# Kernel optimization log

Measured on AMD Instinct MI355X. Metric: run time of the kernel, lower is better.

The kernel has to match this reference:

```python
import jax, jax.numpy as jnp
import numpy as np

NUM_HEADS = 12

def setup_inputs() -> dict:
    key = jax.random.key(0)
    ks = jax.random.split(key, 4)
    B, N, C = 64, 512, 768
    x = jax.random.normal(ks[0], (B, N, C), dtype=jnp.float32)
    qkv_w = jax.random.normal(ks[1], (3 * C, C), dtype=jnp.float32) * 0.02
    proj_w = jax.random.normal(ks[2], (C, C), dtype=jnp.float32) * 0.02
    proj_b = jnp.zeros((C,), dtype=jnp.float32)
    bias_table = jax.random.normal(ks[3], (2 * N - 1, NUM_HEADS), dtype=jnp.float32) * 0.02
    return {"x": x, "qkv_w": qkv_w, "proj_w": proj_w, "proj_b": proj_b, "bias_table": bias_table}

def reference(x, qkv_w, proj_w, proj_b, bias_table):
    B, N, C = x.shape
    H = NUM_HEADS
    hd = C // H
    scale = hd ** (-0.5)
    # qkv projection (no bias): [B,N,3C] -> [3,B,H,N,hd]
    qkv = (x @ qkv_w.T).reshape(B, N, 3, H, hd)
    qkv = jnp.transpose(qkv, (2, 0, 3, 1, 4))
    q, k, v = qkv[0], qkv[1], qkv[2]
    # relative position bias: rel index in [0, 2N-2]
    coords = jnp.arange(N)
    rel = coords[:, None] - coords[None, :] + (N - 1)  # [N,N]
    bias = jnp.transpose(bias_table[rel], (2, 0, 1))   # [H,N,N]
    attn = jnp.einsum('bhnd,bhmd->bhnm', q, k) * scale + bias[None]
    attn = jax.nn.softmax(attn, axis=-1)
    out = jnp.einsum('bhnm,bhmd->bhnd', attn, v)       # [B,H,N,hd]
    out = jnp.transpose(out, (0, 2, 1, 3)).reshape(B, N, C)
    return out @ proj_w.T + proj_b
```

## Files before the change

kernel.cpp:

```cpp
#include <hip/hip_runtime.h>
#include <hip/hip_bf16.h>

#define DI static __device__ __forceinline__

typedef __attribute__((ext_vector_type(8), may_alias)) short short8;
typedef __attribute__((ext_vector_type(4), may_alias)) short short4a;
typedef __attribute__((ext_vector_type(4), may_alias)) float floatx4a;
typedef __attribute__((ext_vector_type(4))) float floatx4;

constexpr int Bsz = 64, Nseq = 512, Cdim = 768, NH = 12, HD = 64;
constexpr int QS = Bsz * NH * Nseq * HD;
constexpr float SCALE = 0.125f;

DI ushort f2bf(float f) {
  union { float f; unsigned u; } v; v.f = f;
  unsigned r = v.u + 0x7FFF + ((v.u >> 16) & 1);
  return (ushort)(r >> 16);
}
DI float bf2f(ushort u) {
  union { unsigned u; float f; } v; v.u = ((unsigned)u) << 16;
  return v.f;
}

__global__ void cvt8(const float* __restrict__ s, ushort* __restrict__ d, int n) {
  int i = (blockIdx.x * 256 + threadIdx.x) * 8;
  if (i >= n) return;
  floatx4a a = *(const floatx4a*)(s + i);
  floatx4a b = *(const floatx4a*)(s + i + 4);
  short8 r;
  r[0] = (short)f2bf(a[0]); r[1] = (short)f2bf(a[1]);
  r[2] = (short)f2bf(a[2]); r[3] = (short)f2bf(a[3]);
  r[4] = (short)f2bf(b[0]); r[5] = (short)f2bf(b[1]);
  r[6] = (short)f2bf(b[2]); r[7] = (short)f2bf(b[3]);
  *(short8*)(d + i) = r;
}
__global__ void cvt1(const float* __restrict__ s, ushort* __restrict__ d, int n) {
  int i = blockIdx.x * 256 + threadIdx.x;
  if (i < n) d[i] = f2bf(s[i]);
}

__global__ __launch_bounds__(256) void qkv_gemm(
    const ushort* __restrict__ x, const ushort* __restrict__ w,
    ushort* __restrict__ qo, ushort* __restrict__ ko, ushort* __restrict__ vo)
{
  __shared__ __align__(16) ushort As[128 * 72];
  __shared__ __align__(16) ushort Ws[128 * 72];
  const int bn = blockIdx.x;
  const int bm = blockIdx.y;
  const int t = threadIdx.x;
  const int wv = t >> 6, ln = t & 63, lq = ln >> 4, lm = ln & 15;
  const int wm = wv >> 1, wn = wv & 1;

  floatx4 acc[4][4];
  #pragma unroll
  for (int i = 0; i < 4; ++i)
    #pragma unroll
    for (int j = 0; j < 4; ++j) acc[i][j] = (floatx4)0.f;

  for (int kt = 0; kt < Cdim / 64; ++kt) {
    #pragma unroll
    for (int i = 0; i < 4; ++i) {
      int id = t + 256 * i;
      int r = id >> 3, c = (id & 7) << 3;
      *(short8*)&As[r * 72 + c] =
          *(const short8*)&x[(size_t)(bm * 128 + r) * Cdim + kt * 64 + c];
      *(short8*)&Ws[r * 72 + c] =
          *(const short8*)&w[(size_t)(bn * 128 + r) * Cdim + kt * 64 + c];
    }
    __syncthreads();
    #pragma unroll
    for (int ks = 0; ks < 2; ++ks) {
      short8 af[4], bfr[4];
      #pragma unroll
      for (int i = 0; i < 4; ++i)
        af[i] = *(const short8*)&As[(wm * 64 + i * 16 + lm) * 72 + ks * 32 + lq * 8];
      #pragma unroll
      for (int j = 0; j < 4; ++j)
        bfr[j] = *(const short8*)&Ws[(wn * 64 + j * 16 + lm) * 72 + ks * 32 + lq * 8];
      #pragma unroll
      for (int i = 0; i < 4; ++i)
        #pragma unroll
        for (int j = 0; j < 4; ++j)
          acc[i][j] = __builtin_amdgcn_mfma_f32_16x16x32_bf16(af[i], bfr[j], acc[i][j], 0, 0, 0);
    }
    __syncthreads();
  }

  const int cbase = bn * 128 + wn * 64;
  const int which = cbase / Cdim;
  const int h = (cbase % Cdim) >> 6;
  #pragma unroll
  for (int i = 0; i < 4; ++i) {
    int gm0 = bm * 128 + wm * 64 + i * 16 + lq * 4;
    int b = gm0 >> 9, ns0 = gm0 & 511;
    #pragma unroll
    for (int j = 0; j < 4; ++j) {
      int d = j * 16 + lm;
      if (which == 2) {
        short4a v4;
        #pragma unroll
        for (int r = 0; r < 4; ++r) v4[r] = (short)f2bf(acc[i][j][r]);
        *(short4a*)&vo[(size_t)((b * NH + h) * HD + d) * Nseq + ns0] = v4;
      } else {
        ushort* outp = which == 0 ? qo : ko;
        #pragma unroll
        for (int r = 0; r < 4; ++r)
          outp[(size_t)((b * NH + h) * Nseq + ns0 + r) * HD + d] = f2bf(acc[i][j][r]);
      }
    }
  }
}

__global__ __launch_bounds__(256) void attn_kernel(
    const ushort* __restrict__ q, const ushort* __restrict__ k,
    const ushort* __restrict__ vt, const ushort* __restrict__ bt,
    ushort* __restrict__ ao)
{
  __shared__ __align__(16) ushort Qs[64 * 72];
  __shared__ __align__(16) ushort Ks[64 * 72];
  __shared__ __align__(16) ushort Vs[64 * 72];
  __shared__ __align__(16) ushort Ps[64 * 72];
  __shared__ float biasLds[128];
  const int blk = blockIdx.x;
  const int bh = blk % (Bsz * NH);
  const int qt = blk / (Bsz * NH);
  const int h = bh % NH, b = bh / NH;
  const int t = threadIdx.x;
  const int wv = t >> 6, ln = t & 63, lq = ln >> 4, lm = ln & 15;
  const size_t base = (size_t)bh * (Nseq * HD);

  #pragma unroll
  for (int i = 0; i < 2; ++i) {
    int id = t + 256 * i;
    int r = id >> 3, c = (id & 7) << 3;
    *(short8*)&Qs[r * 72 + c] =
        *(const short8*)&q[base + (size_t)(qt * 64 + r) * HD + c];
  }

  floatx4 o[4];
  #pragma unroll
  for (int i = 0; i < 4; ++i) o[i] = (floatx4)0.f;
  float mrow[4], lrow[4];
  #pragma unroll
  for (int r = 0; r < 4; ++r) { mrow[r] = -1e30f; lrow[r] = 0.f; }

  for (int kt = 0; kt < Nseq / 64; ++kt) {
    #pragma unroll
    for (int i = 0; i < 2; ++i) {
      int id = t + 256 * i;
      int r = id >> 3, c = (id & 7) << 3;
      *(short8*)&Ks[r * 72 + c] =
          *(const short8*)&k[base + (size_t)(kt * 64 + r) * HD + c];
      *(short8*)&Vs[r * 72 + c] =
          *(const short8*)&vt[base + (size_t)r * Nseq + kt * 64 + c];
    }
    if (t < 127) biasLds[t] = bf2f(bt[(qt * 64 - kt * 64 + 448 + t) * NH + h]);
    __syncthreads();

    floatx4 s[4];
    #pragma unroll
    for (int cb = 0; cb < 4; ++cb) s[cb] = (floatx4)0.f;
    #pragma unroll
    for (int ks = 0; ks < 2; ++ks) {
      short8 a = *(const short8*)&Qs[(wv * 16 + lm) * 72 + ks * 32 + lq * 8];
      #pragma unroll
      for (int cb = 0; cb < 4; ++cb) {
        short8 bfr = *(const short8*)&Ks[(cb * 16 + lm) * 72 + ks * 32 + lq * 8];
        s[cb] = __builtin_amdgcn_mfma_f32_16x16x32_bf16(a, bfr, s[cb], 0, 0, 0);
      }
    }

    float pvals[4][4];
    #pragma unroll
    for (int r = 0; r < 4; ++r) {
      int row_in = wv * 16 + lq * 4 + r;
      float sv[4];
      float vmax = -1e30f;
      #pragma unroll
      for (int cb = 0; cb < 4; ++cb) {
        int col_in = cb * 16 + lm;
        float bias = biasLds[row_in - col_in + 63];
        sv[cb] = s[cb][r] * SCALE + bias;
        vmax = fmaxf(vmax, sv[cb]);
      }
      #pragma unroll
      for (int off = 8; off; off >>= 1) vmax = fmaxf(vmax, __shfl_xor(vmax, off));
      float mnew = fmaxf(mrow[r], vmax);
      float alpha = __expf(mrow[r] - mnew);
      float rsum = 0.f;
      #pragma unroll
      for (int cb = 0; cb < 4; ++cb) {
        float p = __expf(sv[cb] - mnew);
        pvals[cb][r] = p;
        rsum += p;
      }
      #pragma unroll
      for (int off = 8; off; off >>= 1) rsum += __shfl_xor(rsum, off);
      lrow[r] = lrow[r] * alpha + rsum;
      mrow[r] = mnew;
      #pragma unroll
      for (int db = 0; db < 4; ++db) o[db][r] *= alpha;
    }

    #pragma unroll
    for (int cb = 0; cb < 4; ++cb)
      #pragma unroll
      for (int r = 0; r < 4; ++r)
        Ps[(wv * 16 + lq * 4 + r) * 72 + cb * 16 + lm] = f2bf(pvals[cb][r]);

    __syncthreads();

    #pragma unroll
    for (int ks = 0; ks < 2; ++ks) {
      short8 a = *(const short8*)&Ps[(wv * 16 + lm) * 72 + ks * 32 + lq * 8];
      #pragma unroll
      for (int db = 0; db < 4; ++db) {
        short8 bfr = *(const short8*)&Vs[(db * 16 + lm) * 72 + ks * 32 + lq * 8];
        o[db] = __builtin_amdgcn_mfma_f32_16x16x32_bf16(a, bfr, o[db], 0, 0, 0);
      }
    }
    __syncthreads();
  }

  #pragma unroll
  for (int r = 0; r < 4; ++r) {
    int qi = qt * 64 + wv * 16 + lq * 4 + r;
    float inv = 1.f / lrow[r];
    #pragma unroll
    for (int db = 0; db < 4; ++db) {
      int d = db * 16 + lm;
      ao[(size_t)(b * Nseq + qi) * Cdim + h * HD + d] = f2bf(o[db][r] * inv);
    }
  }
}

__global__ __launch_bounds__(256) void proj_gemm(
    const ushort* __restrict__ a, const ushort* __restrict__ w,
    const ushort* __restrict__ pb, float* __restrict__ out)
{
  __shared__ __align__(16) ushort As[128 * 72];
  __shared__ __align__(16) ushort Ws[128 * 72];
  const int bn = blockIdx.x;
  const int bm = blockIdx.y;
  const int t = threadIdx.x;
  const int wv = t >> 6, ln = t & 63, lq = ln >> 4, lm = ln & 15;
  const int wm = wv >> 1, wn = wv & 1;

  floatx4 acc[4][4];
  #pragma unroll
  for (int i = 0; i < 4; ++i)
    #pragma unroll
    for (int j = 0; j < 4; ++j) acc[i][j] = (floatx4)0.f;

  for (int kt = 0; kt < Cdim / 64; ++kt) {
    #pragma unroll
    for (int i = 0; i < 4; ++i) {
      int id = t + 256 * i;
      int r = id >> 3, c = (id & 7) << 3;
      *(short8*)&As[r * 72 + c] =
          *(const short8*)&a[(size_t)(bm * 128 + r) * Cdim + kt * 64 + c];
      *(short8*)&Ws[r * 72 + c] =
          *(const short8*)&w[(size_t)(bn * 128 + r) * Cdim + kt * 64 + c];
    }
    __syncthreads();
    #pragma unroll
    for (int ks = 0; ks < 2; ++ks) {
      short8 af[4], bfr[4];
      #pragma unroll
      for (int i = 0; i < 4; ++i)
        af[i] = *(const short8*)&As[(wm * 64 + i * 16 + lm) * 72 + ks * 32 + lq * 8];
      #pragma unroll
      for (int j = 0; j < 4; ++j)
        bfr[j] = *(const short8*)&Ws[(wn * 64 + j * 16 + lm) * 72 + ks * 32 + lq * 8];
      #pragma unroll
      for (int i = 0; i < 4; ++i)
        #pragma unroll
        for (int j = 0; j < 4; ++j)
          acc[i][j] = __builtin_amdgcn_mfma_f32_16x16x32_bf16(af[i], bfr[j], acc[i][j], 0, 0, 0);
    }
    __syncthreads();
  }

  #pragma unroll
  for (int j = 0; j < 4; ++j) {
    int gn = bn * 128 + wn * 64 + j * 16 + lm;
    float bias = bf2f(pb[gn]);
    #pragma unroll
    for (int i = 0; i < 4; ++i) {
      #pragma unroll
      for (int r = 0; r < 4; ++r) {
        int gm = bm * 128 + wm * 64 + i * 16 + lq * 4 + r;
        out[(size_t)gm * Cdim + gn] = acc[i][j][r] + bias;
      }
    }
  }
}

extern "C" void kernel_launch(void* const* d_in, const int* in_sizes, int n_in,
                              void* d_out, int out_size, void* d_ws, size_t ws_size,
                              hipStream_t stream) {
  const float* x  = (const float*)d_in[0];
  const float* qw = (const float*)d_in[1];
  const float* pw = (const float*)d_in[2];
  const float* pb = (const float*)d_in[3];
  const float* bt = (const float*)d_in[4];
  float* out = (float*)d_out;

  constexpr int NX = Bsz * Nseq * Cdim;
  constexpr int NQW = 3 * Cdim * Cdim;
  constexpr int NPW = Cdim * Cdim;
  constexpr int NBT = (2 * Nseq - 1) * NH;

  ushort* qs  = (ushort*)d_ws;
  ushort* ks  = qs + QS;
  ushort* vts = ks + QS;
  ushort* ao  = vts + QS;
  ushort* xb  = ao;
  ushort* qwb = ao + QS;
  ushort* pwb = qwb + NQW;
  ushort* pbb = pwb + NPW;
  ushort* btb = pbb + Cdim;

  cvt8<<<(NX  + 2047) / 2048, 256, 0, stream>>>(x,  xb,  NX);
  cvt8<<<(NQW + 2047) / 2048, 256, 0, stream>>>(qw, qwb, NQW);
  cvt8<<<(NPW + 2047) / 2048, 256, 0, stream>>>(pw, pwb, NPW);
  cvt8<<<1, 256, 0, stream>>>(pb, pbb, Cdim);
  cvt1<<<(NBT + 255) / 256, 256, 0, stream>>>(bt, btb, NBT);

  qkv_gemm<<<dim3(18, 256), 256, 0, stream>>>(xb, qwb, qs, ks, vts);
  attn_kernel<<<dim3(Bsz * NH * (Nseq / 64)), 256, 0, stream>>>(qs, ks, vts, btb, ao);
  proj_gemm<<<dim3(6, 256), 256, 0, stream>>>(ao, pwb, pbb, out);
}
```

Before: 598.4 us.

## Use direct global-to-LDS loads and XCD-aware block swizzle in GEMMs

```diff
diff --git a/kernel.cpp b/kernel.cpp
--- a/kernel.cpp
+++ b/kernel.cpp
@@ -20,6 +20,12 @@
 DI float bf2f(ushort u) {
   union { unsigned u; float f; } v; v.u = ((unsigned)u) << 16;
   return v.f;
+}
+
+DI void gload_lds16(const ushort* g, ushort* l) {
+  __builtin_amdgcn_global_load_lds(
+      (const __attribute__((address_space(1))) unsigned int*)g,
+      (__attribute__((address_space(3))) unsigned int*)l, 16, 0, 0);
 }
 
 __global__ void cvt8(const float* __restrict__ s, ushort* __restrict__ d, int n) {
@@ -43,14 +49,19 @@
     const ushort* __restrict__ x, const ushort* __restrict__ w,
     ushort* __restrict__ qo, ushort* __restrict__ ko, ushort* __restrict__ vo)
 {
-  __shared__ __align__(16) ushort As[128 * 72];
-  __shared__ __align__(16) ushort Ws[128 * 72];
-  const int bn = blockIdx.x;
-  const int bm = blockIdx.y;
+  __shared__ __align__(16) ushort As[128 * 64];
+  __shared__ __align__(16) ushort Ws[128 * 64];
+  const int id = blockIdx.y * 18 + blockIdx.x;
+  const int swz = (id & 7) * 576 + (id >> 3);
+  const int bm = swz / 18;
+  const int bn = swz % 18;
   const int t = threadIdx.x;
   const int wv = t >> 6, ln = t & 63, lq = ln >> 4, lm = ln & 15;
   const int wm = wv >> 1, wn = wv & 1;
 
+  const int srow = wv * 32 + (ln >> 3);
+  const int scol = (ln & 7) * 8;
+
   floatx4 acc[4][4];
   #pragma unroll
   for (int i = 0; i < 4; ++i)
@@ -60,12 +71,10 @@
   for (int kt = 0; kt < Cdim / 64; ++kt) {
     #pragma unroll
     for (int i = 0; i < 4; ++i) {
-      int id = t + 256 * i;
-      int r = id >> 3, c = (id & 7) << 3;
-      *(short8*)&As[r * 72 + c] =
-          *(const short8*)&x[(size_t)(bm * 128 + r) * Cdim + kt * 64 + c];
-      *(short8*)&Ws[r * 72 + c] =
-          *(const short8*)&w[(size_t)(bn * 128 + r) * Cdim + kt * 64 + c];
+      gload_lds16(&x[(size_t)(bm * 128 + srow + i * 8) * Cdim + kt * 64 + scol],
+                  &As[(wv * 32 + i * 8) * 64]);
+      gload_lds16(&w[(size_t)(bn * 128 + srow + i * 8) * Cdim + kt * 64 + scol],
+                  &Ws[(wv * 32 + i * 8) * 64]);
     }
     __syncthreads();
     #pragma unroll
@@ -73,10 +82,10 @@
       short8 af[4], bfr[4];
       #pragma unroll
       for (int i = 0; i < 4; ++i)
-        af[i] = *(const short8*)&As[(wm * 64 + i * 16 + lm) * 72 + ks * 32 + lq * 8];
+        af[i] = *(const short8*)&As[(wm * 64 + i * 16 + lm) * 64 + ks * 32 + lq * 8];
       #pragma unroll
       for (int j = 0; j < 4; ++j)
-        bfr[j] = *(const short8*)&Ws[(wn * 64 + j * 16 + lm) * 72 + ks * 32 + lq * 8];
+        bfr[j] = *(const short8*)&Ws[(wn * 64 + j * 16 + lm) * 64 + ks * 32 + lq * 8];
       #pragma unroll
       for (int i = 0; i < 4; ++i)
         #pragma unroll
@@ -238,14 +247,19 @@
     const ushort* __restrict__ a, const ushort* __restrict__ w,
     const ushort* __restrict__ pb, float* __restrict__ out)
 {
-  __shared__ __align__(16) ushort As[128 * 72];
-  __shared__ __align__(16) ushort Ws[128 * 72];
-  const int bn = blockIdx.x;
-  const int bm = blockIdx.y;
+  __shared__ __align__(16) ushort As[128 * 64];
+  __shared__ __align__(16) ushort Ws[128 * 64];
+  const int id = blockIdx.y * 6 + blockIdx.x;
+  const int swz = (id & 7) * 192 + (id >> 3);
+  const int bm = swz / 6;
+  const int bn = swz % 6;
   const int t = threadIdx.x;
   const int wv = t >> 6, ln = t & 63, lq = ln >> 4, lm = ln & 15;
   const int wm = wv >> 1, wn = wv & 1;
 
+  const int srow = wv * 32 + (ln >> 3);
+  const int scol = (ln & 7) * 8;
+
   floatx4 acc[4][4];
   #pragma unroll
   for (int i = 0; i < 4; ++i)
@@ -255,12 +269,10 @@
   for (int kt = 0; kt < Cdim / 64; ++kt) {
     #pragma unroll
     for (int i = 0; i < 4; ++i) {
-      int id = t + 256 * i;
-      int r = id >> 3, c = (id & 7) << 3;
-      *(short8*)&As[r * 72 + c] =
-          *(const short8*)&a[(size_t)(bm * 128 + r) * Cdim + kt * 64 + c];
-      *(short8*)&Ws[r * 72 + c] =
-          *(const short8*)&w[(size_t)(bn * 128 + r) * Cdim + kt * 64 + c];
+      gload_lds16(&a[(size_t)(bm * 128 + srow + i * 8) * Cdim + kt * 64 + scol],
+                  &As[(wv * 32 + i * 8) * 64]);
+      gload_lds16(&w[(size_t)(bn * 128 + srow + i * 8) * Cdim + kt * 64 + scol],
+                  &Ws[(wv * 32 + i * 8) * 64]);
     }
     __syncthreads();
     #pragma unroll
@@ -268,10 +280,10 @@
       short8 af[4], bfr[4];
       #pragma unroll
       for (int i = 0; i < 4; ++i)
-        af[i] = *(const short8*)&As[(wm * 64 + i * 16 + lm) * 72 + ks * 32 + lq * 8];
+        af[i] = *(const short8*)&As[(wm * 64 + i * 16 + lm) * 64 + ks * 32 + lq * 8];
       #pragma unroll
       for (int j = 0; j < 4; ++j)
-        bfr[j] = *(const short8*)&Ws[(wn * 64 + j * 16 + lm) * 72 + ks * 32 + lq * 8];
+        bfr[j] = *(const short8*)&Ws[(wn * 64 + j * 16 + lm) * 64 + ks * 32 + lq * 8];
       #pragma unroll
       for (int i = 0; i < 4; ++i)
         #pragma unroll
```

Result: faster. 581.7 us (-2.8%).
